# Kernel tuning notes

Measured on AMD Instinct MI355X. Metric: run time of the kernel, lower is better.

The kernel has to match this reference:

```python
import jax, jax.numpy as jnp
import numpy as np

N = 1024      # n_nodes
S = 32        # state_dim
M = 32        # message_dim
STEPS = 5     # n_steps


def setup_inputs() -> dict:
    key = jax.random.key(0)
    ks = jax.random.split(key, 12)
    w = lambda k, shape: jax.random.normal(k, shape, jnp.float32) * 0.02
    return {
        "J": jax.random.normal(ks[0], (N, N), jnp.float32),
        "b": jax.random.normal(ks[1], (N,), jnp.float32),
        # message_passing MLP (Linear(2S+3->M), Linear(M->M), Linear(M->M))
        "W1": w(ks[2], (M, 2 * S + 3)), "b1": jnp.zeros((M,), jnp.float32),
        "W2": w(ks[3], (M, M)),         "b2": jnp.zeros((M,), jnp.float32),
        "W3": w(ks[4], (M, M)),         "b3": jnp.zeros((M,), jnp.float32),
        # GRU(input=S+M, hidden=S). h0 is always zero in the original forward,
        # so weight_hh never contributes (only bias_hh does) and is omitted.
        "W_ih": w(ks[5], (3 * S, S + M)),
        "b_ih": w(ks[6], (3 * S,)),
        "b_hh": w(ks[7], (3 * S,)),
        # readout MLP (Linear(S->M), Linear(M->M), Linear(M->2))
        "R1": w(ks[8], (M, S)),  "rb1": jnp.zeros((M,), jnp.float32),
        "R2": w(ks[9], (M, M)),  "rb2": jnp.zeros((M,), jnp.float32),
        "R3": w(ks[10], (2, M)), "rb3": jnp.zeros((2,), jnp.float32),
    }


def reference(J, b, W1, b1, W2, b2, W3, b3, W_ih, b_ih, b_hh, R1, rb1, R2, rb2, R3, rb3):
    # Split first linear over the concat [h_i, h_j, J_ij, b_i, b_j] so the
    # [N, N, 2S+3] concat tensor is never materialized.
    W1a, W1b = W1[:, :S], W1[:, S:2 * S]
    wJ, wbi, wbj = W1[:, 2 * S], W1[:, 2 * S + 1], W1[:, 2 * S + 2]

    def step(h, _):
        hi = h @ W1a.T                       # [N, M] (sender part)
        hj = h @ W1b.T                       # [N, M] (receiver part)
        pre = (hi[:, None, :] + hj[None, :, :]
               + J[:, :, None] * wJ
               + b[:, None, None] * wbi
               + b[None, :, None] * wbj
               + b1)                          # [N, N, M]
        x = jax.nn.relu(pre)
        x = jax.nn.relu(x @ W2.T + b2)
        x = jax.nn.relu(x @ W3.T + b3)       # message_i_j: [N, N, M]
        m = x.sum(0)                          # message to node j: sum over senders i
        # GRU with zero initial hidden state: h' = (1-z) * n_gate
        gi = jnp.concatenate([h, m], axis=-1) @ W_ih.T + b_ih  # [N, 3S]
        r = jax.nn.sigmoid(gi[:, :S] + b_hh[:S])
        z = jax.nn.sigmoid(gi[:, S:2 * S] + b_hh[S:2 * S])
        n = jnp.tanh(gi[:, 2 * S:] + r * b_hh[2 * S:])
        return (1.0 - z) * n, None

    h0 = jnp.zeros((N, S), J.dtype)
    h, _ = jax.lax.scan(step, h0, None, length=STEPS)

    r = jax.nn.relu(h @ R1.T + rb1)
    r = jax.nn.relu(r @ R2.T + rb2)
    r = jax.nn.relu(r @ R3.T + rb3)          # [N, 2]
    return jax.nn.sigmoid(r)
```

## Files before the change

kernel.cpp:

```cpp
#include <hip/hip_runtime.h>
#include <hip/hip_cooperative_groups.h>
#include <math.h>

namespace cg = cooperative_groups;

#define NN 1024

typedef __attribute__((ext_vector_type(8))) short bf16x8;
typedef __attribute__((ext_vector_type(4))) float f32x4;
typedef __attribute__((ext_vector_type(4))) unsigned int u32x4;

__device__ __forceinline__ float sigmoidf_(float x) { return 1.0f / (1.0f + __expf(-x)); }

__device__ __forceinline__ unsigned int pk_bf16(float a, float b) {
    unsigned int ua = __float_as_uint(a), ub = __float_as_uint(b);
    ua += 0x7fffu + ((ua >> 16) & 1u);
    ub += 0x7fffu + ((ub >> 16) & 1u);
    return (ua >> 16) | (ub & 0xffff0000u);
}
__device__ __forceinline__ unsigned short f2bf_rne(float a) {
    unsigned int ua = __float_as_uint(a);
    ua += 0x7fffu + ((ua >> 16) & 1u);
    return (unsigned short)(ua >> 16);
}

struct Ctx {
    bf16x8 w2a0, w2a1, w3a0, w3a1;
    f32x4 b2v0, b2v1, b3v0, b3v1;
    float wj8[8];
};

__device__ __forceinline__ void make_ctx(Ctx& c, int p, int q,
    const float* __restrict__ W1, const float* __restrict__ W2,
    const float* __restrict__ b2, const float* __restrict__ W3,
    const float* __restrict__ b3)
{
    union FU { bf16x8 v; unsigned short s[8]; } t0, t1, t2, t3;
#pragma unroll
    for (int jj = 0; jj < 8; jj++) {
        int k = q * 8 + jj;
        t0.s[jj] = f2bf_rne(W2[p * 32 + k]);
        t1.s[jj] = f2bf_rne(W2[(16 + p) * 32 + k]);
        t2.s[jj] = f2bf_rne(W3[p * 32 + k]);
        t3.s[jj] = f2bf_rne(W3[(16 + p) * 32 + k]);
        c.wj8[jj] = W1[k * 67 + 64];
    }
    c.w2a0 = t0.v; c.w2a1 = t1.v; c.w3a0 = t2.v; c.w3a1 = t3.v;
#pragma unroll
    for (int r = 0; r < 4; r++) {
        c.b2v0[r] = b2[q * 4 + r];  c.b2v1[r] = b2[16 + q * 4 + r];
        c.b3v0[r] = b3[q * 4 + r];  c.b3v1[r] = b3[16 + q * 4 + r];
    }
}

__device__ __forceinline__ void tile_op(const Ctx& c,
    const float* __restrict__ Jtrow, const float* __restrict__ u,
    const float* vv, unsigned int* yb, int i, int p, int q,
    f32x4& acc0, f32x4& acc1)
{
    const float jw = Jtrow[i];
    const float4 u0 = *(const float4*)(u + i * 32 + q * 8);
    const float4 u1 = *(const float4*)(u + i * 32 + q * 8 + 4);
    float xr[8];
    xr[0] = fmaxf(fmaf(jw, c.wj8[0], u0.x + vv[0]), 0.f);
    xr[1] = fmaxf(fmaf(jw, c.wj8[1], u0.y + vv[1]), 0.f);
    xr[2] = fmaxf(fmaf(jw, c.wj8[2], u0.z + vv[2]), 0.f);
    xr[3] = fmaxf(fmaf(jw, c.wj8[3], u0.w + vv[3]), 0.f);
    xr[4] = fmaxf(fmaf(jw, c.wj8[4], u1.x + vv[4]), 0.f);
    xr[5] = fmaxf(fmaf(jw, c.wj8[5], u1.y + vv[5]), 0.f);
    xr[6] = fmaxf(fmaf(jw, c.wj8[6], u1.z + vv[6]), 0.f);
    xr[7] = fmaxf(fmaf(jw, c.wj8[7], u1.w + vv[7]), 0.f);

    union BU { u32x4 u4; bf16x8 v; unsigned int d[4]; } bx;
#pragma unroll
    for (int cc = 0; cc < 4; cc++) bx.d[cc] = pk_bf16(xr[2 * cc], xr[2 * cc + 1]);

    f32x4 c0 = __builtin_amdgcn_mfma_f32_16x16x32_bf16(c.w2a0, bx.v, c.b2v0, 0, 0, 0);
    f32x4 c1 = __builtin_amdgcn_mfma_f32_16x16x32_bf16(c.w2a1, bx.v, c.b2v1, 0, 0, 0);

    yb[p * 20 + q * 2 + 0]     = pk_bf16(fmaxf(c0[0], 0.f), fmaxf(c0[1], 0.f));
    yb[p * 20 + q * 2 + 1]     = pk_bf16(fmaxf(c0[2], 0.f), fmaxf(c0[3], 0.f));
    yb[p * 20 + 8 + q * 2 + 0] = pk_bf16(fmaxf(c1[0], 0.f), fmaxf(c1[1], 0.f));
    yb[p * 20 + 8 + q * 2 + 1] = pk_bf16(fmaxf(c1[2], 0.f), fmaxf(c1[3], 0.f));

    union BU yrd;
    yrd.u4 = *(const u32x4*)(yb + p * 20 + q * 4);

    f32x4 e0 = __builtin_amdgcn_mfma_f32_16x16x32_bf16(c.w3a0, yrd.v, c.b3v0, 0, 0, 0);
    f32x4 e1 = __builtin_amdgcn_mfma_f32_16x16x32_bf16(c.w3a1, yrd.v, c.b3v1, 0, 0, 0);
#pragma unroll
    for (int r = 0; r < 4; r++) {
        acc0[r] += fmaxf(e0[r], 0.f);
        acc1[r] += fmaxf(e1[r], 0.f);
    }
}

__device__ __forceinline__ void gru_row(int s, float hval, float mval, float bj,
    const float* __restrict__ Wih, const float* __restrict__ bih,
    const float* __restrict__ bhh, const float* __restrict__ W1,
    const float* __restrict__ b1, float& hn, float& uacc, float& vacc)
{
    float g0 = bih[s], g1 = bih[32 + s], g2 = bih[64 + s];
#pragma unroll 8
    for (int k = 0; k < 32; k++) {
        float hk = __shfl(hval, k, 32);
        float mk = __shfl(mval, k, 32);
        g0 = fmaf(Wih[s * 64 + k],             hk, g0);
        g0 = fmaf(Wih[s * 64 + 32 + k],        mk, g0);
        g1 = fmaf(Wih[(32 + s) * 64 + k],      hk, g1);
        g1 = fmaf(Wih[(32 + s) * 64 + 32 + k], mk, g1);
        g2 = fmaf(Wih[(64 + s) * 64 + k],      hk, g2);
        g2 = fmaf(Wih[(64 + s) * 64 + 32 + k], mk, g2);
    }
    float r = sigmoidf_(g0 + bhh[s]);
    float z = sigmoidf_(g1 + bhh[32 + s]);
    float n = tanhf(g2 + r * bhh[64 + s]);
    hn = (1.0f - z) * n;
    float ua = bj * W1[s * 67 + 65];
    float va = fmaf(bj, W1[s * 67 + 66], b1[s]);
#pragma unroll 8
    for (int k = 0; k < 32; k++) {
        float hk = __shfl(hn, k, 32);
        ua = fmaf(W1[s * 67 + k],      hk, ua);
        va = fmaf(W1[s * 67 + 32 + k], hk, va);
    }
    uacc = ua; vacc = va;
}

__device__ __forceinline__ void readout_row(int s, int j, float hn,
    const float* __restrict__ R1, const float* __restrict__ rb1,
    const float* __restrict__ R2, const float* __restrict__ rb2,
    const float* __restrict__ R3, const float* __restrict__ rb3,
    float* __restrict__ out)
{
    float a1 = rb1[s];
#pragma unroll 8
    for (int k = 0; k < 32; k++) a1 = fmaf(R1[s * 32 + k], __shfl(hn, k, 32), a1);
    a1 = fmaxf(a1, 0.f);
    float a2 = rb2[s];
#pragma unroll 8
    for (int k = 0; k < 32; k++) a2 = fmaf(R2[s * 32 + k], __shfl(a1, k, 32), a2);
    a2 = fmaxf(a2, 0.f);
    float a3 = (s < 2) ? rb3[s] : 0.f;
#pragma unroll 8
    for (int k = 0; k < 32; k++) {
        float a2k = __shfl(a2, k, 32);
        if (s < 2) a3 = fmaf(R3[s * 32 + k], a2k, a3);
    }
    if (s < 2) out[j * 2 + s] = sigmoidf_(fmaxf(a3, 0.f));
}

__global__ __launch_bounds__(256) void k_pre(
    const float* __restrict__ J, const float* __restrict__ b,
    const float* __restrict__ W1, const float* __restrict__ b1,
    float* __restrict__ Jt, float* __restrict__ h,
    float* __restrict__ u0, float* __restrict__ v)
{
    __shared__ float tile[32][33];
    const int t = blockIdx.x;
    const int tid = threadIdx.x;
    if (t < 1024) {
        int tx = (t & 31) * 32, ty = (t >> 5) * 32;
        int x = tid & 31, y = tid >> 5;
#pragma unroll
        for (int r = 0; r < 4; r++)
            tile[y + 8 * r][x] = J[(size_t)(ty + y + 8 * r) * NN + tx + x];
        __syncthreads();
#pragma unroll
        for (int r = 0; r < 4; r++)
            Jt[(size_t)(tx + y + 8 * r) * NN + ty + x] = tile[x][y + 8 * r];
    } else {
        int idx = (t - 1024) * 256 + tid;
        int row = idx >> 5, mm = idx & 31;
        float bi = b[row];
        h[idx]  = 0.f;
        u0[idx] = bi * W1[mm * 67 + 65];
        v[idx]  = fmaf(bi, W1[mm * 67 + 66], b1[mm]);
    }
}

__global__ __launch_bounds__(128, 2) void k_coop(
    const float* __restrict__ Jt, const float* __restrict__ W1,
    const float* __restrict__ W2, const float* __restrict__ b2,
    const float* __restrict__ W3, const float* __restrict__ b3,
    const float* __restrict__ Wih, const float* __restrict__ bih,
    const float* __restrict__ bhh, const float* __restrict__ b,
    const float* __restrict__ b1,
    const float* __restrict__ R1, const float* __restrict__ rb1,
    const float* __restrict__ R2, const float* __restrict__ rb2,
    const float* __restrict__ R3, const float* __restrict__ rb3,
    const float* __restrict__ vin, float* __restrict__ u0,
    float* __restrict__ u1, float* __restrict__ out)
{
    __shared__ unsigned int ybuf[2 * 4 * 320];
    __shared__ float red[2 * 32];
    __shared__ float hbuf[32], vbuf[32];

    const int tid = threadIdx.x;
    const int w = tid >> 6;
    const int l = tid & 63;
    const int p = l & 15;
    const int q = l >> 4;
    const int j = blockIdx.x;

    Ctx c; make_ctx(c, p, q, W1, W2, b2, W3, b3);
    const float* Jtrow = Jt + (size_t)j * NN;

    if (tid < 32) { hbuf[tid] = 0.f; vbuf[tid] = vin[j * 32 + tid]; }
    __syncthreads();

    for (int step = 0; step < 5; ++step) {
        const float* ui = (step & 1) ? u1 : u0;
        float*       uo = (step & 1) ? u0 : u1;

        float vv[8];
#pragma unroll
        for (int jj = 0; jj < 8; jj++) vv[jj] = vbuf[q * 8 + jj];

        f32x4 acc0 = {0.f, 0.f, 0.f, 0.f}, acc1 = {0.f, 0.f, 0.f, 0.f};
#pragma unroll 4
        for (int t = 0; t < 32; ++t)
            tile_op(c, Jtrow, ui, vv, ybuf + w * 1280 + (t & 3) * 320,
                    w * 512 + t * 16 + p, p, q, acc0, acc1);

#pragma unroll
        for (int bit = 1; bit < 16; bit <<= 1) {
#pragma unroll
            for (int r = 0; r < 4; r++) {
                acc0[r] += __shfl_xor(acc0[r], bit);
                acc1[r] += __shfl_xor(acc1[r], bit);
            }
        }
        if (p == 0) {
#pragma unroll
            for (int r = 0; r < 4; r++) {
                red[w * 32 + q * 4 + r]      = acc0[r];
                red[w * 32 + 16 + q * 4 + r] = acc1[r];
            }
        }
        __syncthreads();

        if (tid < 32) {
            const int s = tid;
            float mval = red[s] + red[32 + s];
            float hn, ua, va;
            gru_row(s, hbuf[s], mval, b[j], Wih, bih, bhh, W1, b1, hn, ua, va);
            hbuf[s] = hn; vbuf[s] = va;
            uo[j * 32 + s] = ua;
            if (step == 4) readout_row(s, j, hn, R1, rb1, R2, rb2, R3, rb3, out);
        }
        if (step < 4) { __threadfence(); cg::this_grid().sync(); }
    }
}

__global__ __launch_bounds__(256, 4) void k_step(
    const float* __restrict__ Jt, const float* __restrict__ W1,
    const float* __restrict__ W2, const float* __restrict__ b2,
    const float* __restrict__ W3, const float* __restrict__ b3,
    const float* __restrict__ Wih, const float* __restrict__ bih,
    const float* __restrict__ bhh, const float* __restrict__ b,
    const float* __restrict__ b1,
    const float* __restrict__ R1, const float* __restrict__ rb1,
    const float* __restrict__ R2, const float* __restrict__ rb2,
    const float* __restrict__ R3, const float* __restrict__ rb3,
    float* __restrict__ h, float* __restrict__ v,
    const float* __restrict__ ui, float* __restrict__ uo,
    float* __restrict__ out, int do_out)
{
    __shared__ unsigned int ybuf[4 * 2 * 320];
    __shared__ float red[4 * 32];

    const int tid = threadIdx.x;
    const int w = tid >> 6;
    const int l = tid & 63;
    const int p = l & 15;
    const int q = l >> 4;
    const int j = blockIdx.x;

    Ctx c; make_ctx(c, p, q, W1, W2, b2, W3, b3);
    const float* Jtrow = Jt + (size_t)j * NN;

    float vv[8];
#pragma unroll
    for (int jj = 0; jj < 8; jj++) vv[jj] = v[j * 32 + q * 8 + jj];

    f32x4 acc0 = {0.f, 0.f, 0.f, 0.f}, acc1 = {0.f, 0.f, 0.f, 0.f};
#pragma unroll 2
    for (int t = 0; t < 16; ++t)
        tile_op(c, Jtrow, ui, vv, ybuf + w * 640 + (t & 1) * 320,
                w * 256 + t * 16 + p, p, q, acc0, acc1);

#pragma unroll
    for (int bit = 1; bit < 16; bit <<= 1) {
#pragma unroll
        for (int r = 0; r < 4; r++) {
            acc0[r] += __shfl_xor(acc0[r], bit);
            acc1[r] += __shfl_xor(acc1[r], bit);
        }
    }
    if (p == 0) {
#pragma unroll
        for (int r = 0; r < 4; r++) {
            red[w * 32 + q * 4 + r]      = acc0[r];
            red[w * 32 + 16 + q * 4 + r] = acc1[r];
        }
    }
    __syncthreads();

    if (tid < 32) {
        const int s = tid;
        float mval = red[s] + red[32 + s] + red[64 + s] + red[96 + s];
        float hn, ua, va;
        gru_row(s, h[j * 32 + s], mval, b[j], Wih, bih, bhh, W1, b1, hn, ua, va);
        h[j * 32 + s] = hn;
        v[j * 32 + s] = va;
        uo[j * 32 + s] = ua;
        if (do_out) readout_row(s, j, hn, R1, rb1, R2, rb2, R3, rb3, out);
    }
}

extern "C" void kernel_launch(void* const* d_in, const int* in_sizes, int n_in,
                              void* d_out, int out_size, void* d_ws, size_t ws_size,
                              hipStream_t stream)
{
    const float* J   = (const float*)d_in[0];
    const float* b   = (const float*)d_in[1];
    const float* W1  = (const float*)d_in[2];
    const float* b1  = (const float*)d_in[3];
    const float* W2  = (const float*)d_in[4];
    const float* b2  = (const float*)d_in[5];
    const float* W3  = (const float*)d_in[6];
    const float* b3  = (const float*)d_in[7];
    const float* Wih = (const float*)d_in[8];
    const float* bih = (const float*)d_in[9];
    const float* bhh = (const float*)d_in[10];
    const float* R1  = (const float*)d_in[11];
    const float* rb1 = (const float*)d_in[12];
    const float* R2  = (const float*)d_in[13];
    const float* rb2 = (const float*)d_in[14];
    const float* R3  = (const float*)d_in[15];
    const float* rb3 = (const float*)d_in[16];

    float* out = (float*)d_out;
    float* ws  = (float*)d_ws;
    float* h  = ws;
    float* v  = ws + 32768;
    float* u0 = ws + 65536;
    float* u1 = ws + 98304;
    float* Jt = ws + 131072;

    k_pre<<<1152, 256, 0, stream>>>(J, b, W1, b1, Jt, h, u0, v);

    int mb = 0;
    bool coop =
        (hipOccupancyMaxActiveBlocksPerMultiprocessor(
             &mb, reinterpret_cast<const void*>(&k_coop), 128, 0) == hipSuccess) &&
        (mb >= 4);
    if (coop) {
        const float* vin = v;
        void* cargs[] = { (void*)&Jt, (void*)&W1, (void*)&W2, (void*)&b2,
                          (void*)&W3, (void*)&b3, (void*)&Wih, (void*)&bih,
                          (void*)&bhh, (void*)&b, (void*)&b1,
                          (void*)&R1, (void*)&rb1, (void*)&R2, (void*)&rb2,
                          (void*)&R3, (void*)&rb3,
                          (void*)&vin, (void*)&u0, (void*)&u1, (void*)&out };
        if (hipLaunchCooperativeKernel(reinterpret_cast<const void*>(&k_coop),
                                       dim3(1024), dim3(128), cargs, 0, stream)
            != hipSuccess)
            coop = false;
    }
    if (!coop) {
        for (int s = 0; s < 5; s++) {
            const float* ui = (s & 1) ? u1 : u0;
            float*       uo = (s & 1) ? u0 : u1;
            k_step<<<1024, 256, 0, stream>>>(Jt, W1, W2, b2, W3, b3, Wih, bih,
                                             bhh, b, b1, R1, rb1, R2, rb2, R3,
                                             rb3, h, v, ui, uo, out,
                                             (s == 4) ? 1 : 0);
        }
    }
}
```

Baseline: 224.5 us.

## Drop cooperative grid-sync kernel; use per-step launches with register prefetch

Removes the persistent cooperative kernel that ran all five steps with grid-wide syncs, and always launches one k_step kernel per message-passing step. The step kernel's tile loop is inlined and software-pipelined: the J value and u vectors for the next tile are loaded into registers while the current tile is computed. This trades grid-sync overhead and the cooperative occupancy limits for extra kernel launches plus reloading h/v from global memory each step.

```diff
diff --git a/kernel.cpp b/kernel.cpp
--- a/kernel.cpp
+++ b/kernel.cpp
@@ -1,8 +1,5 @@
 #include <hip/hip_runtime.h>
-#include <hip/hip_cooperative_groups.h>
 #include <math.h>
-
-namespace cg = cooperative_groups;
 
 #define NN 1024
 
@@ -50,48 +47,6 @@
     for (int r = 0; r < 4; r++) {
         c.b2v0[r] = b2[q * 4 + r];  c.b2v1[r] = b2[16 + q * 4 + r];
         c.b3v0[r] = b3[q * 4 + r];  c.b3v1[r] = b3[16 + q * 4 + r];
-    }
-}
-
-__device__ __forceinline__ void tile_op(const Ctx& c,
-    const float* __restrict__ Jtrow, const float* __restrict__ u,
-    const float* vv, unsigned int* yb, int i, int p, int q,
-    f32x4& acc0, f32x4& acc1)
-{
-    const float jw = Jtrow[i];
-    const float4 u0 = *(const float4*)(u + i * 32 + q * 8);
-    const float4 u1 = *(const float4*)(u + i * 32 + q * 8 + 4);
-    float xr[8];
-    xr[0] = fmaxf(fmaf(jw, c.wj8[0], u0.x + vv[0]), 0.f);
-    xr[1] = fmaxf(fmaf(jw, c.wj8[1], u0.y + vv[1]), 0.f);
-    xr[2] = fmaxf(fmaf(jw, c.wj8[2], u0.z + vv[2]), 0.f);
-    xr[3] = fmaxf(fmaf(jw, c.wj8[3], u0.w + vv[3]), 0.f);
-    xr[4] = fmaxf(fmaf(jw, c.wj8[4], u1.x + vv[4]), 0.f);
-    xr[5] = fmaxf(fmaf(jw, c.wj8[5], u1.y + vv[5]), 0.f);
-    xr[6] = fmaxf(fmaf(jw, c.wj8[6], u1.z + vv[6]), 0.f);
-    xr[7] = fmaxf(fmaf(jw, c.wj8[7], u1.w + vv[7]), 0.f);
-
-    union BU { u32x4 u4; bf16x8 v; unsigned int d[4]; } bx;
-#pragma unroll
-    for (int cc = 0; cc < 4; cc++) bx.d[cc] = pk_bf16(xr[2 * cc], xr[2 * cc + 1]);
-
-    f32x4 c0 = __builtin_amdgcn_mfma_f32_16x16x32_bf16(c.w2a0, bx.v, c.b2v0, 0, 0, 0);
-    f32x4 c1 = __builtin_amdgcn_mfma_f32_16x16x32_bf16(c.w2a1, bx.v, c.b2v1, 0, 0, 0);
-
-    yb[p * 20 + q * 2 + 0]     = pk_bf16(fmaxf(c0[0], 0.f), fmaxf(c0[1], 0.f));
-    yb[p * 20 + q * 2 + 1]     = pk_bf16(fmaxf(c0[2], 0.f), fmaxf(c0[3], 0.f));
-    yb[p * 20 + 8 + q * 2 + 0] = pk_bf16(fmaxf(c1[0], 0.f), fmaxf(c1[1], 0.f));
-    yb[p * 20 + 8 + q * 2 + 1] = pk_bf16(fmaxf(c1[2], 0.f), fmaxf(c1[3], 0.f));
-
-    union BU yrd;
-    yrd.u4 = *(const u32x4*)(yb + p * 20 + q * 4);
-
-    f32x4 e0 = __builtin_amdgcn_mfma_f32_16x16x32_bf16(c.w3a0, yrd.v, c.b3v0, 0, 0, 0);
-    f32x4 e1 = __builtin_amdgcn_mfma_f32_16x16x32_bf16(c.w3a1, yrd.v, c.b3v1, 0, 0, 0);
-#pragma unroll
-    for (int r = 0; r < 4; r++) {
-        acc0[r] += fmaxf(e0[r], 0.f);
-        acc1[r] += fmaxf(e1[r], 0.f);
     }
 }
 
@@ -176,80 +131,6 @@
         h[idx]  = 0.f;
         u0[idx] = bi * W1[mm * 67 + 65];
         v[idx]  = fmaf(bi, W1[mm * 67 + 66], b1[mm]);
-    }
-}
-
-__global__ __launch_bounds__(128, 2) void k_coop(
-    const float* __restrict__ Jt, const float* __restrict__ W1,
-    const float* __restrict__ W2, const float* __restrict__ b2,
-    const float* __restrict__ W3, const float* __restrict__ b3,
-    const float* __restrict__ Wih, const float* __restrict__ bih,
-    const float* __restrict__ bhh, const float* __restrict__ b,
-    const float* __restrict__ b1,
-    const float* __restrict__ R1, const float* __restrict__ rb1,
-    const float* __restrict__ R2, const float* __restrict__ rb2,
-    const float* __restrict__ R3, const float* __restrict__ rb3,
-    const float* __restrict__ vin, float* __restrict__ u0,
-    float* __restrict__ u1, float* __restrict__ out)
-{
-    __shared__ unsigned int ybuf[2 * 4 * 320];
-    __shared__ float red[2 * 32];
-    __shared__ float hbuf[32], vbuf[32];
-
-    const int tid = threadIdx.x;
-    const int w = tid >> 6;
-    const int l = tid & 63;
-    const int p = l & 15;
-    const int q = l >> 4;
-    const int j = blockIdx.x;
-
-    Ctx c; make_ctx(c, p, q, W1, W2, b2, W3, b3);
-    const float* Jtrow = Jt + (size_t)j * NN;
-
-    if (tid < 32) { hbuf[tid] = 0.f; vbuf[tid] = vin[j * 32 + tid]; }
-    __syncthreads();
-
-    for (int step = 0; step < 5; ++step) {
-        const float* ui = (step & 1) ? u1 : u0;
-        float*       uo = (step & 1) ? u0 : u1;
-
-        float vv[8];
-#pragma unroll
-        for (int jj = 0; jj < 8; jj++) vv[jj] = vbuf[q * 8 + jj];
-
-        f32x4 acc0 = {0.f, 0.f, 0.f, 0.f}, acc1 = {0.f, 0.f, 0.f, 0.f};
-#pragma unroll 4
-        for (int t = 0; t < 32; ++t)
-            tile_op(c, Jtrow, ui, vv, ybuf + w * 1280 + (t & 3) * 320,
-                    w * 512 + t * 16 + p, p, q, acc0, acc1);
-
-#pragma unroll
-        for (int bit = 1; bit < 16; bit <<= 1) {
-#pragma unroll
-            for (int r = 0; r < 4; r++) {
-                acc0[r] += __shfl_xor(acc0[r], bit);
-                acc1[r] += __shfl_xor(acc1[r], bit);
-            }
-        }
-        if (p == 0) {
-#pragma unroll
-            for (int r = 0; r < 4; r++) {
-                red[w * 32 + q * 4 + r]      = acc0[r];
-                red[w * 32 + 16 + q * 4 + r] = acc1[r];
-            }
-        }
-        __syncthreads();
-
-        if (tid < 32) {
-            const int s = tid;
-            float mval = red[s] + red[32 + s];
-            float hn, ua, va;
-            gru_row(s, hbuf[s], mval, b[j], Wih, bih, bhh, W1, b1, hn, ua, va);
-            hbuf[s] = hn; vbuf[s] = va;
-            uo[j * 32 + s] = ua;
-            if (step == 4) readout_row(s, j, hn, R1, rb1, R2, rb2, R3, rb3, out);
-        }
-        if (step < 4) { __threadfence(); cg::this_grid().sync(); }
     }
 }
 
@@ -285,10 +166,58 @@
     for (int jj = 0; jj < 8; jj++) vv[jj] = v[j * 32 + q * 8 + jj];
 
     f32x4 acc0 = {0.f, 0.f, 0.f, 0.f}, acc1 = {0.f, 0.f, 0.f, 0.f};
+
+    int i0 = w * 256 + p;
+    float  jw = Jtrow[i0];
+    float4 ua = *(const float4*)(ui + i0 * 32 + q * 8);
+    float4 ub = *(const float4*)(ui + i0 * 32 + q * 8 + 4);
+
 #pragma unroll 2
-    for (int t = 0; t < 16; ++t)
-        tile_op(c, Jtrow, ui, vv, ybuf + w * 640 + (t & 1) * 320,
-                w * 256 + t * 16 + p, p, q, acc0, acc1);
+    for (int t = 0; t < 16; ++t) {
+        const float  jw_c = jw;
+        const float4 ua_c = ua;
+        const float4 ub_c = ub;
+        if (t < 15) {
+            const int in = w * 256 + (t + 1) * 16 + p;
+            jw = Jtrow[in];
+            ua = *(const float4*)(ui + in * 32 + q * 8);
+            ub = *(const float4*)(ui + in * 32 + q * 8 + 4);
+        }
+
+        float xr[8];
+        xr[0] = fmaxf(fmaf(jw_c, c.wj8[0], ua_c.x + vv[0]), 0.f);
+        xr[1] = fmaxf(fmaf(jw_c, c.wj8[1], ua_c.y + vv[1]), 0.f);
+        xr[2] = fmaxf(fmaf(jw_c, c.wj8[2], ua_c.z + vv[2]), 0.f);
+        xr[3] = fmaxf(fmaf(jw_c, c.wj8[3], ua_c.w + vv[3]), 0.f);
+        xr[4] = fmaxf(fmaf(jw_c, c.wj8[4], ub_c.x + vv[4]), 0.f);
+        xr[5] = fmaxf(fmaf(jw_c, c.wj8[5], ub_c.y + vv[5]), 0.f);
+        xr[6] = fmaxf(fmaf(jw_c, c.wj8[6], ub_c.z + vv[6]), 0.f);
+        xr[7] = fmaxf(fmaf(jw_c, c.wj8[7], ub_c.w + vv[7]), 0.f);
+
+        union BU { u32x4 u4; bf16x8 v; unsigned int d[4]; } bx;
+#pragma unroll
+        for (int cc = 0; cc < 4; cc++) bx.d[cc] = pk_bf16(xr[2 * cc], xr[2 * cc + 1]);
+
+        f32x4 c0 = __builtin_amdgcn_mfma_f32_16x16x32_bf16(c.w2a0, bx.v, c.b2v0, 0, 0, 0);
+        f32x4 c1 = __builtin_amdgcn_mfma_f32_16x16x32_bf16(c.w2a1, bx.v, c.b2v1, 0, 0, 0);
+
+        unsigned int* yb = ybuf + w * 640 + (t & 1) * 320;
+        yb[p * 20 + q * 2 + 0]     = pk_bf16(fmaxf(c0[0], 0.f), fmaxf(c0[1], 0.f));
+        yb[p * 20 + q * 2 + 1]     = pk_bf16(fmaxf(c0[2], 0.f), fmaxf(c0[3], 0.f));
+        yb[p * 20 + 8 + q * 2 + 0] = pk_bf16(fmaxf(c1[0], 0.f), fmaxf(c1[1], 0.f));
+        yb[p * 20 + 8 + q * 2 + 1] = pk_bf16(fmaxf(c1[2], 0.f), fmaxf(c1[3], 0.f));
+
+        union BU yrd;
+        yrd.u4 = *(const u32x4*)(yb + p * 20 + q * 4);
+
+        f32x4 e0 = __builtin_amdgcn_mfma_f32_16x16x32_bf16(c.w3a0, yrd.v, c.b3v0, 0, 0, 0);
+        f32x4 e1 = __builtin_amdgcn_mfma_f32_16x16x32_bf16(c.w3a1, yrd.v, c.b3v1, 0, 0, 0);
+#pragma unroll
+        for (int r = 0; r < 4; r++) {
+            acc0[r] += fmaxf(e0[r], 0.f);
+            acc1[r] += fmaxf(e1[r], 0.f);
+        }
+    }
 
 #pragma unroll
     for (int bit = 1; bit < 16; bit <<= 1) {
@@ -310,11 +239,11 @@
     if (tid < 32) {
         const int s = tid;
         float mval = red[s] + red[32 + s] + red[64 + s] + red[96 + s];
-        float hn, ua, va;
-        gru_row(s, h[j * 32 + s], mval, b[j], Wih, bih, bhh, W1, b1, hn, ua, va);
+        float hn, uacc, vacc;
+        gru_row(s, h[j * 32 + s], mval, b[j], Wih, bih, bhh, W1, b1, hn, uacc, vacc);
         h[j * 32 + s] = hn;
-        v[j * 32 + s] = va;
-        uo[j * 32 + s] = ua;
+        v[j * 32 + s] = vacc;
+        uo[j * 32 + s] = uacc;
         if (do_out) readout_row(s, j, hn, R1, rb1, R2, rb2, R3, rb3, out);
     }
 }
@@ -350,33 +279,12 @@
     float* Jt = ws + 131072;
 
     k_pre<<<1152, 256, 0, stream>>>(J, b, W1, b1, Jt, h, u0, v);
-
-    int mb = 0;
-    bool coop =
-        (hipOccupancyMaxActiveBlocksPerMultiprocessor(
-             &mb, reinterpret_cast<const void*>(&k_coop), 128, 0) == hipSuccess) &&
-        (mb >= 4);
-    if (coop) {
-        const float* vin = v;
-        void* cargs[] = { (void*)&Jt, (void*)&W1, (void*)&W2, (void*)&b2,
-                          (void*)&W3, (void*)&b3, (void*)&Wih, (void*)&bih,
-                          (void*)&bhh, (void*)&b, (void*)&b1,
-                          (void*)&R1, (void*)&rb1, (void*)&R2, (void*)&rb2,
-                          (void*)&R3, (void*)&rb3,
-                          (void*)&vin, (void*)&u0, (void*)&u1, (void*)&out };
-        if (hipLaunchCooperativeKernel(reinterpret_cast<const void*>(&k_coop),
-                                       dim3(1024), dim3(128), cargs, 0, stream)
-            != hipSuccess)
-            coop = false;
-    }
-    if (!coop) {
-        for (int s = 0; s < 5; s++) {
-            const float* ui = (s & 1) ? u1 : u0;
-            float*       uo = (s & 1) ? u0 : u1;
-            k_step<<<1024, 256, 0, stream>>>(Jt, W1, W2, b2, W3, b3, Wih, bih,
-                                             bhh, b, b1, R1, rb1, R2, rb2, R3,
-                                             rb3, h, v, ui, uo, out,
-                                             (s == 4) ? 1 : 0);
-        }
-    }
-}
+    for (int s = 0; s < 5; s++) {
+        const float* ui = (s & 1) ? u1 : u0;
+        float*       uo = (s & 1) ? u0 : u1;
+        k_step<<<1024, 256, 0, stream>>>(Jt, W1, W2, b2, W3, b3, Wih, bih,
+                                         bhh, b, b1, R1, rb1, R2, rb2, R3,
+                                         rb3, h, v, ui, uo, out,
+                                         (s == 4) ? 1 : 0);
+    }
+}
```

New measurement: 225.0 us. No clear change (+0.2%).
